# Kernel tuning notes

Hardware: AMD Instinct MI355X
Metric: run time of the kernel (lower is better)

## Reference

```python
import jax, jax.numpy as jnp
import numpy as np

N = 262144  # IMU samples
M = 2048    # synced keyframe poses
GRAVITY = 9.81007

# ---- quaternion helpers (pypose xyzw convention) ----

def qmul(q, r):
    x1, y1, z1, w1 = q[..., 0:1], q[..., 1:2], q[..., 2:3], q[..., 3:4]
    x2, y2, z2, w2 = r[..., 0:1], r[..., 1:2], r[..., 2:3], r[..., 3:4]
    return jnp.concatenate([
        w1 * x2 + x1 * w2 + y1 * z2 - z1 * y2,
        w1 * y2 - x1 * z2 + y1 * w2 + z1 * x2,
        w1 * z2 + x1 * y2 - y1 * x2 + z1 * w2,
        w1 * w2 - x1 * x2 - y1 * y2 - z1 * z2,
    ], axis=-1)


def qconj(q):
    return q * jnp.array([-1.0, -1.0, -1.0, 1.0], dtype=q.dtype)


def qrot(q, v):
    # rotate vector v by unit quaternion q
    xyz, w = q[..., :3], q[..., 3:4]
    t = 2.0 * jnp.cross(xyz, v)
    return v + w * t + jnp.cross(xyz, t)


def exp_so3(phi):
    # axis-angle -> unit quaternion (xyzw); jnp.sinc is safe at 0
    theta = jnp.linalg.norm(phi, axis=-1, keepdims=True)
    half = 0.5 * theta
    xyz = phi * (0.5 * jnp.sinc(half / jnp.pi))  # sin(half)/theta
    w = jnp.cos(half)
    return jnp.concatenate([xyz, w], axis=-1)


def log_so3(q):
    # unit quaternion -> axis-angle vector
    xyz, w = q[..., :3], q[..., 3:4]
    nn = jnp.linalg.norm(xyz, axis=-1, keepdims=True)
    theta = 2.0 * jnp.arctan2(nn, w)
    nn_safe = jnp.maximum(nn, 1e-12)
    scale = jnp.where(nn < 1e-7, 2.0, theta / nn_safe)  # small-angle: ~2*xyz
    return xyz * scale


def preintegrate(accels, gyros, dts, q0, v0, p0):
    """Sequential IMU preintegration (rotation at interval start rotates acc)."""
    grav = jnp.array([0.0, 0.0, -GRAVITY], dtype=accels.dtype)
    dt = dts[:, 0]  # [N]

    def step(carry, inp):
        q, v, p = carry
        w_m, a_m, dti = inp
        a_world = qrot(q, a_m) + grav
        p_new = p + v * dti + 0.5 * a_world * dti * dti
        v_new = v + a_world * dti
        q_new = qmul(q, exp_so3(w_m * dti))
        q_new = q_new / jnp.linalg.norm(q_new)
        return (q_new, v_new, p_new), (q_new, p_new)

    _, (rots, poss) = jax.lax.scan(step, (q0, v0, p0), (gyros, accels, dt))
    return rots, poss  # [N,4], [N,3]


def setup_inputs() -> dict:
    key = jax.random.key(0)
    ks = jax.random.split(key, 11)
    accels = 0.5 * jax.random.normal(ks[0], (N, 3), jnp.float32) \
             + jnp.array([0.0, 0.0, GRAVITY], jnp.float32)
    gyros = 0.1 * jax.random.normal(ks[1], (N, 3), jnp.float32)
    accel_bias = 0.01 * jax.random.normal(ks[2], (3,), jnp.float32)
    gyro_bias = 0.001 * jax.random.normal(ks[3], (3,), jnp.float32)
    dts = 0.004 + 0.002 * jax.random.uniform(ks[4], (N, 1), jnp.float32)  # ~200Hz
    init_rot = jax.random.normal(ks[5], (4,), jnp.float32)
    init_rot = init_rot / jnp.linalg.norm(init_rot)
    init_pos = 0.1 * jax.random.normal(ks[6], (3,), jnp.float32)
    init_vel = 0.1 * jax.random.normal(ks[7], (3,), jnp.float32)
    poses_rot = jax.random.normal(ks[8], (M, 4), jnp.float32)
    poses_rot = poses_rot / jnp.linalg.norm(poses_rot, axis=-1, keepdims=True)
    poses_trans = 10.0 * jax.random.normal(ks[9], (M, 3), jnp.float32)
    sync = jnp.sort(jax.random.randint(ks[10], (M,), 0, N))
    return {"accels": accels, "gyros": gyros, "accel_bias": accel_bias,
            "gyro_bias": gyro_bias, "dts": dts, "init_rot": init_rot,
            "init_pos": init_pos, "init_vel": init_vel,
            "poses_rot": poses_rot, "poses_trans": poses_trans, "sync": sync}


def reference(accels, gyros, accel_bias, gyro_bias, dts, init_rot, init_pos,
              init_vel, poses_rot, poses_trans, sync):
    acc = accels - accel_bias[None, :]
    gyr = gyros - gyro_bias[None, :]
    rots, poss = preintegrate(acc, gyr, dts, init_rot, init_vel, init_pos)
    rot_s = rots[sync]   # [M,4]
    pos_s = poss[sync]   # [M,3]
    rel = qmul(qconj(poses_rot), rot_s)
    roterr = jnp.linalg.norm(log_so3(rel))              # global Frobenius norm
    transerr = jnp.mean((poses_trans - pos_s) ** 2)     # mse_loss
    return roterr + transerr
```

## Files before the change

### kernel.cpp

```cpp
#include <hip/hip_runtime.h>
#include <math.h>

#define NN   262144
#define MM   2048
#define SUB  16
#define BT   64
#define SPB  (BT * SUB)
#define NB1  (NN / SPB)
#define NTH  (NN / SUB)
#define REC  113
#define GRAV 9.81007f

struct Qt { float x, y, z, w; };
struct V3 { float x, y, z; };

__device__ __forceinline__ V3 v3(float x, float y, float z) { V3 r{x, y, z}; return r; }
__device__ __forceinline__ V3 vadd(V3 a, V3 b) { return v3(a.x + b.x, a.y + b.y, a.z + b.z); }
__device__ __forceinline__ V3 vscale(V3 a, float s) { return v3(a.x * s, a.y * s, a.z * s); }
__device__ __forceinline__ float vdot(V3 a, V3 b) { return a.x * b.x + a.y * b.y + a.z * b.z; }

__device__ __forceinline__ Qt qmul(Qt a, Qt b) {
    Qt r;
    r.x = a.w * b.x + a.x * b.w + a.y * b.z - a.z * b.y;
    r.y = a.w * b.y - a.x * b.z + a.y * b.w + a.z * b.x;
    r.z = a.w * b.z + a.x * b.y - a.y * b.x + a.z * b.w;
    r.w = a.w * b.w - a.x * b.x - a.y * b.y - a.z * b.z;
    return r;
}
__device__ __forceinline__ Qt qnorm(Qt a) {
    float rn = rsqrtf(a.x * a.x + a.y * a.y + a.z * a.z + a.w * a.w);
    Qt r{a.x * rn, a.y * rn, a.z * rn, a.w * rn};
    return r;
}
__device__ __forceinline__ V3 qrot(Qt q, V3 v) {
    float tx = 2.f * (q.y * v.z - q.z * v.y);
    float ty = 2.f * (q.z * v.x - q.x * v.z);
    float tz = 2.f * (q.x * v.y - q.y * v.x);
    V3 r;
    r.x = v.x + q.w * tx + (q.y * tz - q.z * ty);
    r.y = v.y + q.w * ty + (q.z * tx - q.x * tz);
    r.z = v.z + q.w * tz + (q.x * ty - q.y * tx);
    return r;
}
__device__ __forceinline__ Qt exp_so3(V3 phi) {
    float t2 = vdot(phi, phi);
    float th = sqrtf(t2);
    float h = 0.5f * th;
    float s, c;
    if (h < 0.1f) {
        float h2 = h * h;
        s = 0.5f * (1.f - h2 * (1.f / 6.f) + h2 * h2 * (1.f / 120.f));
        c = 1.f - h2 * 0.5f + h2 * h2 * (1.f / 24.f);
    } else {
        s = 0.5f * sinf(h) / h;
        c = cosf(h);
    }
    Qt r{phi.x * s, phi.y * s, phi.z * s, c};
    return r;
}

__device__ __forceinline__ void step_state(Qt& q, V3& v, V3& p, V3 a, V3 w, float dt) {
    V3 aw = qrot(q, a);
    aw.z -= GRAV;
    float hdt2 = 0.5f * dt * dt;
    p.x += v.x * dt + aw.x * hdt2;
    p.y += v.y * dt + aw.y * hdt2;
    p.z += v.z * dt + aw.z * hdt2;
    v.x += aw.x * dt;
    v.y += aw.y * dt;
    v.z += aw.z * dt;
    q = qnorm(qmul(q, exp_so3(v3(w.x * dt, w.y * dt, w.z * dt))));
}

struct Sm { Qt q; float T; V3 B1; V3 C; float W; };

__device__ __forceinline__ Sm sm_identity() {
    Sm s; s.q = Qt{0, 0, 0, 1}; s.T = 0; s.B1 = v3(0, 0, 0); s.C = v3(0, 0, 0); s.W = 0; return s;
}
__device__ __forceinline__ Sm sm_combine(const Sm& a, const Sm& b) {
    Sm r;
    r.q  = qnorm(qmul(a.q, b.q));
    r.T  = a.T + b.T;
    r.B1 = vadd(a.B1, qrot(a.q, b.B1));
    r.C  = vadd(vadd(a.C, vscale(a.B1, b.T)), qrot(a.q, b.C));
    r.W  = a.W + a.T * b.T + b.W;
    return r;
}
__device__ __forceinline__ void sm_store(float* p, const Sm& s) {
    p[0] = s.q.x; p[1] = s.q.y; p[2] = s.q.z; p[3] = s.q.w;
    p[4] = s.T;
    p[5] = s.B1.x; p[6] = s.B1.y; p[7] = s.B1.z;
    p[8] = s.C.x;  p[9] = s.C.y;  p[10] = s.C.z;
    p[11] = s.W;
}
__device__ __forceinline__ Sm sm_load(const float* p) {
    Sm s;
    s.q = Qt{p[0], p[1], p[2], p[3]};
    s.T = p[4];
    s.B1 = v3(p[5], p[6], p[7]);
    s.C  = v3(p[8], p[9], p[10]);
    s.W = p[11];
    return s;
}
__device__ __forceinline__ Sm sm_shfl_up(const Sm& s, int off) {
    Sm r;
    r.q.x = __shfl_up(s.q.x, off); r.q.y = __shfl_up(s.q.y, off);
    r.q.z = __shfl_up(s.q.z, off); r.q.w = __shfl_up(s.q.w, off);
    r.T = __shfl_up(s.T, off);
    r.B1.x = __shfl_up(s.B1.x, off); r.B1.y = __shfl_up(s.B1.y, off); r.B1.z = __shfl_up(s.B1.z, off);
    r.C.x = __shfl_up(s.C.x, off);  r.C.y = __shfl_up(s.C.y, off);  r.C.z = __shfl_up(s.C.z, off);
    r.W = __shfl_up(s.W, off);
    return r;
}

struct St { Qt q; V3 v; V3 p; };
__device__ __forceinline__ St apply_sm(const Sm& P, Qt q0, V3 v0, V3 p0) {
    St s;
    s.q = qnorm(qmul(q0, P.q));
    V3 vb = qrot(q0, P.B1);
    V3 pb = qrot(q0, P.C);
    s.v = v3(v0.x + vb.x, v0.y + vb.y, v0.z + vb.z - GRAV * P.T);
    s.p = v3(p0.x + v0.x * P.T + pb.x,
             p0.y + v0.y * P.T + pb.y,
             p0.z + v0.z * P.T + pb.z - GRAV * P.W);
    return s;
}
__device__ __forceinline__ void st_store(float* p, const St& s) {
    p[0] = s.q.x; p[1] = s.q.y; p[2] = s.q.z; p[3] = s.q.w;
    p[4] = s.v.x; p[5] = s.v.y; p[6] = s.v.z;
    p[7] = s.p.x; p[8] = s.p.y; p[9] = s.p.z;
}
__device__ __forceinline__ St st_load(const float* p) {
    St s;
    s.q = Qt{p[0], p[1], p[2], p[3]};
    s.v = v3(p[4], p[5], p[6]);
    s.p = v3(p[7], p[8], p[9]);
    return s;
}

__global__ __launch_bounds__(BT) void k_sum(
    const float* __restrict__ acc, const float* __restrict__ gyr,
    const float* __restrict__ ab, const float* __restrict__ gb,
    const float* __restrict__ dts,
    float* __restrict__ prefix, float* __restrict__ blocksums) {
    __shared__ float lds[BT * REC];
    int b = blockIdx.x;
    int t = threadIdx.x;

    const float4* ga = (const float4*)(acc + (size_t)b * SPB * 3);
    const float4* gg = (const float4*)(gyr + (size_t)b * SPB * 3);
    const float4* gd = (const float4*)(dts + (size_t)b * SPB);
#pragma unroll
    for (int r = 0; r < 12; ++r) {
        int i4 = r * BT + t;
        float4 v = ga[i4];
        int i = i4 * 4;
        float* d = &lds[(i / 48) * REC + (i % 48)];
        d[0] = v.x; d[1] = v.y; d[2] = v.z; d[3] = v.w;
    }
#pragma unroll
    for (int r = 0; r < 12; ++r) {
        int i4 = r * BT + t;
        float4 v = gg[i4];
        int i = i4 * 4;
        float* d = &lds[(i / 48) * REC + 48 + (i % 48)];
        d[0] = v.x; d[1] = v.y; d[2] = v.z; d[3] = v.w;
    }
#pragma unroll
    for (int r = 0; r < 4; ++r) {
        int i4 = r * BT + t;
        float4 v = gd[i4];
        int i = i4 * 4;
        float* d = &lds[(i / 16) * REC + 96 + (i % 16)];
        d[0] = v.x; d[1] = v.y; d[2] = v.z; d[3] = v.w;
    }
    __syncthreads();

    float ab0 = ab[0], ab1 = ab[1], ab2 = ab[2];
    float gb0 = gb[0], gb1 = gb[1], gb2 = gb[2];

    const float* rec = &lds[t * REC];
    Qt q{0.f, 0.f, 0.f, 1.f};
    V3 B1 = v3(0, 0, 0), B2 = v3(0, 0, 0);
    float tt = 0.f, U = 0.f;
#pragma unroll
    for (int j = 0; j < SUB; ++j) {
        V3 a = v3(rec[3 * j] - ab0, rec[3 * j + 1] - ab1, rec[3 * j + 2] - ab2);
        V3 w = v3(rec[48 + 3 * j] - gb0, rec[48 + 3 * j + 1] - gb1, rec[48 + 3 * j + 2] - gb2);
        float dt = rec[96 + j];
        V3 bb = qrot(q, a);
        float tc = tt + 0.5f * dt;
        B1 = vadd(B1, vscale(bb, dt));
        B2 = vadd(B2, vscale(bb, dt * tc));
        U += dt * tc;
        tt += dt;
        q = qnorm(qmul(q, exp_so3(v3(w.x * dt, w.y * dt, w.z * dt))));
    }
    Sm cur;
    cur.q = q; cur.T = tt; cur.B1 = B1;
    cur.C = vadd(vscale(B1, tt), vscale(B2, -1.f));
    cur.W = tt * tt - U;

#pragma unroll
    for (int off = 1; off < 64; off <<= 1) {
        Sm o = sm_shfl_up(cur, off);
        if (t >= off) cur = sm_combine(o, cur);
    }
    sm_store(prefix + (size_t)(b * BT + t) * 12, cur);
    if (t == BT - 1) sm_store(blocksums + (size_t)b * 12, cur);
}

__global__ __launch_bounds__(NB1) void k_scan(
    const float* __restrict__ blocksums,
    const float* __restrict__ q0p, const float* __restrict__ p0p, const float* __restrict__ v0p,
    float* __restrict__ S, float* __restrict__ accum) {
    __shared__ float ls[NB1][12];
    int tid = threadIdx.x;
    Sm cur = sm_load(blocksums + (size_t)tid * 12);
    sm_store(ls[tid], cur);
    for (int off = 1; off < NB1; off <<= 1) {
        __syncthreads();
        Sm t = sm_load(ls[tid]);
        if (tid >= off) t = sm_combine(sm_load(ls[tid - off]), t);
        __syncthreads();
        sm_store(ls[tid], t);
    }
    __syncthreads();
    Qt q0{q0p[0], q0p[1], q0p[2], q0p[3]};
    V3 p0 = v3(p0p[0], p0p[1], p0p[2]);
    V3 v0 = v3(v0p[0], v0p[1], v0p[2]);
    Sm incl = sm_load(ls[tid]);
    St s = apply_sm(incl, q0, v0, p0);
    st_store(S + (size_t)(tid + 1) * 12, s);
    if (tid == 0) {
        St s0; s0.q = qnorm(q0); s0.v = v0; s0.p = p0;
        st_store(S, s0);
        accum[0] = 0.f; accum[1] = 0.f;
    }
}

__global__ __launch_bounds__(64) void k_sync(
    const float* __restrict__ acc, const float* __restrict__ gyr,
    const float* __restrict__ ab, const float* __restrict__ gb,
    const float* __restrict__ dts,
    const float* __restrict__ prefix, const float* __restrict__ S,
    const float* __restrict__ prot, const float* __restrict__ ptrn,
    const int* __restrict__ sync, float* __restrict__ accum) {
    int m = blockIdx.x * blockDim.x + threadIdx.x;
    float rsq = 0.f, tsq = 0.f;
    if (m < MM) {
        int g = sync[m] + 1;
        int b = g >> 10;
        int t = (g >> 4) & (BT - 1);
        int r = g & (SUB - 1);
        St st = st_load(S + (size_t)b * 12);
        if (t > 0) {
            Sm P = sm_load(prefix + (size_t)(b * BT + t - 1) * 12);
            st = apply_sm(P, st.q, st.v, st.p);
        }
        if (r > 0) {
            float ab0 = ab[0], ab1 = ab[1], ab2 = ab[2];
            float gb0 = gb[0], gb1 = gb[1], gb2 = gb[2];
            int base = g & ~(SUB - 1);
            for (int j = 0; j < r; ++j) {
                int i = base + j;
                V3 a = v3(acc[3 * i] - ab0, acc[3 * i + 1] - ab1, acc[3 * i + 2] - ab2);
                V3 w = v3(gyr[3 * i] - gb0, gyr[3 * i + 1] - gb1, gyr[3 * i + 2] - gb2);
                step_state(st.q, st.v, st.p, a, w, dts[i]);
            }
        }
        Qt pr{prot[4 * m], prot[4 * m + 1], prot[4 * m + 2], prot[4 * m + 3]};
        Qt pc{-pr.x, -pr.y, -pr.z, pr.w};
        Qt rel = qmul(pc, st.q);
        float nn = sqrtf(rel.x * rel.x + rel.y * rel.y + rel.z * rel.z);
        float theta = 2.f * atan2f(nn, rel.w);
        float scale = (nn < 1e-7f) ? 2.f : theta / fmaxf(nn, 1e-12f);
        float lx = rel.x * scale, ly = rel.y * scale, lz = rel.z * scale;
        rsq = lx * lx + ly * ly + lz * lz;
        float dx = ptrn[3 * m] - st.p.x, dy = ptrn[3 * m + 1] - st.p.y, dz = ptrn[3 * m + 2] - st.p.z;
        tsq = dx * dx + dy * dy + dz * dz;
    }
    for (int o = 32; o > 0; o >>= 1) {
        rsq += __shfl_down(rsq, o);
        tsq += __shfl_down(tsq, o);
    }
    if ((threadIdx.x & 63) == 0) {
        atomicAdd(&accum[0], rsq);
        atomicAdd(&accum[1], tsq);
    }
}

__global__ void k_fin(const float* __restrict__ accum, float* __restrict__ out) {
    out[0] = sqrtf(accum[0]) + accum[1] * (1.f / (3.f * MM));
}

extern "C" void kernel_launch(void* const* d_in, const int* in_sizes, int n_in,
                              void* d_out, int out_size, void* d_ws, size_t ws_size,
                              hipStream_t stream) {
    const float* acc  = (const float*)d_in[0];
    const float* gyr  = (const float*)d_in[1];
    const float* ab   = (const float*)d_in[2];
    const float* gb   = (const float*)d_in[3];
    const float* dts  = (const float*)d_in[4];
    const float* q0   = (const float*)d_in[5];
    const float* p0   = (const float*)d_in[6];
    const float* v0   = (const float*)d_in[7];
    const float* prot = (const float*)d_in[8];
    const float* ptrn = (const float*)d_in[9];
    const int*   sync = (const int*)d_in[10];

    float* ws     = (float*)d_ws;
    float* prefix = ws;
    float* bsums  = prefix + (size_t)NTH * 12;
    float* S      = bsums + (size_t)NB1 * 12;
    float* accum  = S + (size_t)(NB1 + 1) * 12;
    float* out    = (float*)d_out;

    hipLaunchKernelGGL(k_sum, dim3(NB1), dim3(BT), 0, stream,
                       acc, gyr, ab, gb, dts, prefix, bsums);
    hipLaunchKernelGGL(k_scan, dim3(1), dim3(NB1), 0, stream,
                       bsums, q0, p0, v0, S, accum);
    hipLaunchKernelGGL(k_sync, dim3(MM / 64), dim3(64), 0, stream,
                       acc, gyr, ab, gb, dts, prefix, S, prot, ptrn, sync, accum);
    hipLaunchKernelGGL(k_fin, dim3(1), dim3(1), 0, stream, accum, out);
}
```

Before: 104.4 us.

## Fuse scan, sync-pose evaluation and final reduction into one tail kernel

Merges the block-sum scan, the per-keyframe state reconstruction and the final loss kernel into a single 256-thread block. Block-boundary states now stay in shared memory and the result is reduced in-block, so the global atomics and two kernel launches go away. Quaternion renormalisation is also dropped from each inner step and from the scan combine, normalising only once per 16-sample chunk. The trade-off is that the 2048 keyframes are handled by one block (8 per thread) instead of 32 blocks, and skipping normalisation may cause small numerical drift.

New measurement: 166.9 us. 1.6x slower.

```diff
diff --git a/kernel.cpp b/kernel.cpp
--- a/kernel.cpp
+++ b/kernel.cpp
@@ -74,12 +74,9 @@
 
 struct Sm { Qt q; float T; V3 B1; V3 C; float W; };
 
-__device__ __forceinline__ Sm sm_identity() {
-    Sm s; s.q = Qt{0, 0, 0, 1}; s.T = 0; s.B1 = v3(0, 0, 0); s.C = v3(0, 0, 0); s.W = 0; return s;
-}
 __device__ __forceinline__ Sm sm_combine(const Sm& a, const Sm& b) {
     Sm r;
-    r.q  = qnorm(qmul(a.q, b.q));
+    r.q  = qmul(a.q, b.q);
     r.T  = a.T + b.T;
     r.B1 = vadd(a.B1, qrot(a.q, b.B1));
     r.C  = vadd(vadd(a.C, vscale(a.B1, b.T)), qrot(a.q, b.C));
@@ -194,10 +191,10 @@
         B2 = vadd(B2, vscale(bb, dt * tc));
         U += dt * tc;
         tt += dt;
-        q = qnorm(qmul(q, exp_so3(v3(w.x * dt, w.y * dt, w.z * dt))));
+        q = qmul(q, exp_so3(v3(w.x * dt, w.y * dt, w.z * dt)));
     }
     Sm cur;
-    cur.q = q; cur.T = tt; cur.B1 = B1;
+    cur.q = qnorm(q); cur.T = tt; cur.B1 = B1;
     cur.C = vadd(vscale(B1, tt), vscale(B2, -1.f));
     cur.W = tt * tt - U;
 
@@ -210,12 +207,19 @@
     if (t == BT - 1) sm_store(blocksums + (size_t)b * 12, cur);
 }
 
-__global__ __launch_bounds__(NB1) void k_scan(
-    const float* __restrict__ blocksums,
+__global__ __launch_bounds__(NB1) void k_tail(
+    const float* __restrict__ blocksums, const float* __restrict__ prefix,
+    const float* __restrict__ acc, const float* __restrict__ gyr,
+    const float* __restrict__ ab, const float* __restrict__ gb,
+    const float* __restrict__ dts,
     const float* __restrict__ q0p, const float* __restrict__ p0p, const float* __restrict__ v0p,
-    float* __restrict__ S, float* __restrict__ accum) {
+    const float* __restrict__ prot, const float* __restrict__ ptrn,
+    const int* __restrict__ sync, float* __restrict__ out) {
     __shared__ float ls[NB1][12];
+    __shared__ float Sst[NB1 + 1][12];
+    __shared__ float red_r[4], red_t[4];
     int tid = threadIdx.x;
+
     Sm cur = sm_load(blocksums + (size_t)tid * 12);
     sm_store(ls[tid], cur);
     for (int off = 1; off < NB1; off <<= 1) {
@@ -226,41 +230,34 @@
         sm_store(ls[tid], t);
     }
     __syncthreads();
+
     Qt q0{q0p[0], q0p[1], q0p[2], q0p[3]};
     V3 p0 = v3(p0p[0], p0p[1], p0p[2]);
     V3 v0 = v3(v0p[0], v0p[1], v0p[2]);
-    Sm incl = sm_load(ls[tid]);
-    St s = apply_sm(incl, q0, v0, p0);
-    st_store(S + (size_t)(tid + 1) * 12, s);
+    St s = apply_sm(sm_load(ls[tid]), q0, v0, p0);
+    st_store(Sst[tid + 1], s);
     if (tid == 0) {
         St s0; s0.q = qnorm(q0); s0.v = v0; s0.p = p0;
-        st_store(S, s0);
-        accum[0] = 0.f; accum[1] = 0.f;
-    }
-}
-
-__global__ __launch_bounds__(64) void k_sync(
-    const float* __restrict__ acc, const float* __restrict__ gyr,
-    const float* __restrict__ ab, const float* __restrict__ gb,
-    const float* __restrict__ dts,
-    const float* __restrict__ prefix, const float* __restrict__ S,
-    const float* __restrict__ prot, const float* __restrict__ ptrn,
-    const int* __restrict__ sync, float* __restrict__ accum) {
-    int m = blockIdx.x * blockDim.x + threadIdx.x;
+        st_store(Sst[0], s0);
+    }
+    __syncthreads();
+
+    float ab0 = ab[0], ab1 = ab[1], ab2 = ab[2];
+    float gb0 = gb[0], gb1 = gb[1], gb2 = gb[2];
     float rsq = 0.f, tsq = 0.f;
-    if (m < MM) {
+#pragma unroll
+    for (int k = 0; k < MM / NB1; ++k) {
+        int m = k * NB1 + tid;
         int g = sync[m] + 1;
         int b = g >> 10;
         int t = (g >> 4) & (BT - 1);
         int r = g & (SUB - 1);
-        St st = st_load(S + (size_t)b * 12);
+        St st = st_load(Sst[b]);
         if (t > 0) {
             Sm P = sm_load(prefix + (size_t)(b * BT + t - 1) * 12);
             st = apply_sm(P, st.q, st.v, st.p);
         }
         if (r > 0) {
-            float ab0 = ab[0], ab1 = ab[1], ab2 = ab[2];
-            float gb0 = gb[0], gb1 = gb[1], gb2 = gb[2];
             int base = g & ~(SUB - 1);
             for (int j = 0; j < r; ++j) {
                 int i = base + j;
@@ -276,22 +273,21 @@
         float theta = 2.f * atan2f(nn, rel.w);
         float scale = (nn < 1e-7f) ? 2.f : theta / fmaxf(nn, 1e-12f);
         float lx = rel.x * scale, ly = rel.y * scale, lz = rel.z * scale;
-        rsq = lx * lx + ly * ly + lz * lz;
+        rsq += lx * lx + ly * ly + lz * lz;
         float dx = ptrn[3 * m] - st.p.x, dy = ptrn[3 * m + 1] - st.p.y, dz = ptrn[3 * m + 2] - st.p.z;
-        tsq = dx * dx + dy * dy + dz * dz;
+        tsq += dx * dx + dy * dy + dz * dz;
     }
     for (int o = 32; o > 0; o >>= 1) {
         rsq += __shfl_down(rsq, o);
         tsq += __shfl_down(tsq, o);
     }
-    if ((threadIdx.x & 63) == 0) {
-        atomicAdd(&accum[0], rsq);
-        atomicAdd(&accum[1], tsq);
-    }
-}
-
-__global__ void k_fin(const float* __restrict__ accum, float* __restrict__ out) {
-    out[0] = sqrtf(accum[0]) + accum[1] * (1.f / (3.f * MM));
+    if ((tid & 63) == 0) { red_r[tid >> 6] = rsq; red_t[tid >> 6] = tsq; }
+    __syncthreads();
+    if (tid == 0) {
+        float R = red_r[0] + red_r[1] + red_r[2] + red_r[3];
+        float T = red_t[0] + red_t[1] + red_t[2] + red_t[3];
+        out[0] = sqrtf(R) + T * (1.f / (3.f * MM));
+    }
 }
 
 extern "C" void kernel_launch(void* const* d_in, const int* in_sizes, int n_in,
@@ -312,15 +308,11 @@
     float* ws     = (float*)d_ws;
     float* prefix = ws;
     float* bsums  = prefix + (size_t)NTH * 12;
-    float* S      = bsums + (size_t)NB1 * 12;
-    float* accum  = S + (size_t)(NB1 + 1) * 12;
     float* out    = (float*)d_out;
 
     hipLaunchKernelGGL(k_sum, dim3(NB1), dim3(BT), 0, stream,
                        acc, gyr, ab, gb, dts, prefix, bsums);
-    hipLaunchKernelGGL(k_scan, dim3(1), dim3(NB1), 0, stream,
-                       bsums, q0, p0, v0, S, accum);
-    hipLaunchKernelGGL(k_sync, dim3(MM / 64), dim3(64), 0, stream,
-                       acc, gyr, ab, gb, dts, prefix, S, prot, ptrn, sync, accum);
-    hipLaunchKernelGGL(k_fin, dim3(1), dim3(1), 0, stream, accum, out);
-}
+    hipLaunchKernelGGL(k_tail, dim3(1), dim3(NB1), 0, stream,
+                       bsums, prefix, acc, gyr, ab, gb, dts,
+                       q0, p0, v0, prot, ptrn, sync, out);
+}
```

## Parallelize sync-point tail integration with 16-lane segmented scan

Applied to the files above, without the earlier changes.

The per-keyframe sequential tail loop of up to 15 IMU steps is replaced by 16 lanes per keyframe. Each lane builds a one-sample summary element, and the lanes combine them with a shuffle-based scan before one lane applies the result to the block state. Quaternion renormalization is also dropped from the combine and from the per-sample loop in the summary kernel, leaving a single normalization at the end of each thread's chunk. This cuts serial latency in the sync kernel and some arithmetic in the scans, at the cost of 16x more threads in the sync kernel and possible slight numerical drift.

New measurement: 107.8 us. 3.3% more time.

```diff
diff --git a/kernel.cpp b/kernel.cpp
--- a/kernel.cpp
+++ b/kernel.cpp
@@ -59,32 +59,19 @@
     return r;
 }
 
-__device__ __forceinline__ void step_state(Qt& q, V3& v, V3& p, V3 a, V3 w, float dt) {
-    V3 aw = qrot(q, a);
-    aw.z -= GRAV;
-    float hdt2 = 0.5f * dt * dt;
-    p.x += v.x * dt + aw.x * hdt2;
-    p.y += v.y * dt + aw.y * hdt2;
-    p.z += v.z * dt + aw.z * hdt2;
-    v.x += aw.x * dt;
-    v.y += aw.y * dt;
-    v.z += aw.z * dt;
-    q = qnorm(qmul(q, exp_so3(v3(w.x * dt, w.y * dt, w.z * dt))));
-}
-
 struct Sm { Qt q; float T; V3 B1; V3 C; float W; };
 
-__device__ __forceinline__ Sm sm_identity() {
-    Sm s; s.q = Qt{0, 0, 0, 1}; s.T = 0; s.B1 = v3(0, 0, 0); s.C = v3(0, 0, 0); s.W = 0; return s;
-}
 __device__ __forceinline__ Sm sm_combine(const Sm& a, const Sm& b) {
     Sm r;
-    r.q  = qnorm(qmul(a.q, b.q));
+    r.q  = qmul(a.q, b.q);
     r.T  = a.T + b.T;
     r.B1 = vadd(a.B1, qrot(a.q, b.B1));
     r.C  = vadd(vadd(a.C, vscale(a.B1, b.T)), qrot(a.q, b.C));
     r.W  = a.W + a.T * b.T + b.W;
     return r;
+}
+__device__ __forceinline__ Sm sm_identity() {
+    Sm s; s.q = Qt{0, 0, 0, 1}; s.T = 0; s.B1 = v3(0, 0, 0); s.C = v3(0, 0, 0); s.W = 0; return s;
 }
 __device__ __forceinline__ void sm_store(float* p, const Sm& s) {
     p[0] = s.q.x; p[1] = s.q.y; p[2] = s.q.z; p[3] = s.q.w;
@@ -194,10 +181,10 @@
         B2 = vadd(B2, vscale(bb, dt * tc));
         U += dt * tc;
         tt += dt;
-        q = qnorm(qmul(q, exp_so3(v3(w.x * dt, w.y * dt, w.z * dt))));
+        q = qmul(q, exp_so3(v3(w.x * dt, w.y * dt, w.z * dt)));
     }
     Sm cur;
-    cur.q = q; cur.T = tt; cur.B1 = B1;
+    cur.q = qnorm(q); cur.T = tt; cur.B1 = B1;
     cur.C = vadd(vscale(B1, tt), vscale(B2, -1.f));
     cur.W = tt * tt - U;
 
@@ -229,8 +216,7 @@
     Qt q0{q0p[0], q0p[1], q0p[2], q0p[3]};
     V3 p0 = v3(p0p[0], p0p[1], p0p[2]);
     V3 v0 = v3(v0p[0], v0p[1], v0p[2]);
-    Sm incl = sm_load(ls[tid]);
-    St s = apply_sm(incl, q0, v0, p0);
+    St s = apply_sm(sm_load(ls[tid]), q0, v0, p0);
     st_store(S + (size_t)(tid + 1) * 12, s);
     if (tid == 0) {
         St s0; s0.q = qnorm(q0); s0.v = v0; s0.p = p0;
@@ -240,51 +226,69 @@
 }
 
 __global__ __launch_bounds__(64) void k_sync(
+    const float* __restrict__ prefix, const float* __restrict__ S,
     const float* __restrict__ acc, const float* __restrict__ gyr,
     const float* __restrict__ ab, const float* __restrict__ gb,
     const float* __restrict__ dts,
-    const float* __restrict__ prefix, const float* __restrict__ S,
     const float* __restrict__ prot, const float* __restrict__ ptrn,
     const int* __restrict__ sync, float* __restrict__ accum) {
-    int m = blockIdx.x * blockDim.x + threadIdx.x;
+    int tid = blockIdx.x * 64 + threadIdx.x;
+    int m = tid >> 4;
+    int j = tid & 15;
+
+    int g = sync[m] + 1;
+    int b = g >> 10;
+    int t = (g >> 4) & (BT - 1);
+    int r = g & (SUB - 1);
+
+    St st = st_load(S + (size_t)b * 12);
+    if (t > 0) {
+        Sm P = sm_load(prefix + (size_t)(b * BT + t - 1) * 12);
+        st = apply_sm(P, st.q, st.v, st.p);
+    }
+
+    Sm s;
+    if (j < r) {
+        int i = (g & ~(SUB - 1)) + j;
+        float ab0 = ab[0], ab1 = ab[1], ab2 = ab[2];
+        float gb0 = gb[0], gb1 = gb[1], gb2 = gb[2];
+        V3 a = v3(acc[3 * i] - ab0, acc[3 * i + 1] - ab1, acc[3 * i + 2] - ab2);
+        V3 w = v3(gyr[3 * i] - gb0, gyr[3 * i + 1] - gb1, gyr[3 * i + 2] - gb2);
+        float dt = dts[i];
+        s.q = exp_so3(v3(w.x * dt, w.y * dt, w.z * dt));
+        s.T = dt;
+        s.B1 = vscale(a, dt);
+        s.C  = vscale(a, 0.5f * dt * dt);
+        s.W  = 0.5f * dt * dt;
+    } else {
+        s = sm_identity();
+    }
+
+#pragma unroll
+    for (int off = 1; off < 16; off <<= 1) {
+        Sm o = sm_shfl_up(s, off);
+        if (j >= off) s = sm_combine(o, s);
+    }
+
     float rsq = 0.f, tsq = 0.f;
-    if (m < MM) {
-        int g = sync[m] + 1;
-        int b = g >> 10;
-        int t = (g >> 4) & (BT - 1);
-        int r = g & (SUB - 1);
-        St st = st_load(S + (size_t)b * 12);
-        if (t > 0) {
-            Sm P = sm_load(prefix + (size_t)(b * BT + t - 1) * 12);
-            st = apply_sm(P, st.q, st.v, st.p);
-        }
-        if (r > 0) {
-            float ab0 = ab[0], ab1 = ab[1], ab2 = ab[2];
-            float gb0 = gb[0], gb1 = gb[1], gb2 = gb[2];
-            int base = g & ~(SUB - 1);
-            for (int j = 0; j < r; ++j) {
-                int i = base + j;
-                V3 a = v3(acc[3 * i] - ab0, acc[3 * i + 1] - ab1, acc[3 * i + 2] - ab2);
-                V3 w = v3(gyr[3 * i] - gb0, gyr[3 * i + 1] - gb1, gyr[3 * i + 2] - gb2);
-                step_state(st.q, st.v, st.p, a, w, dts[i]);
-            }
-        }
+    if (j == 15) {
+        St f = apply_sm(s, st.q, st.v, st.p);
         Qt pr{prot[4 * m], prot[4 * m + 1], prot[4 * m + 2], prot[4 * m + 3]};
         Qt pc{-pr.x, -pr.y, -pr.z, pr.w};
-        Qt rel = qmul(pc, st.q);
+        Qt rel = qmul(pc, f.q);
         float nn = sqrtf(rel.x * rel.x + rel.y * rel.y + rel.z * rel.z);
         float theta = 2.f * atan2f(nn, rel.w);
         float scale = (nn < 1e-7f) ? 2.f : theta / fmaxf(nn, 1e-12f);
         float lx = rel.x * scale, ly = rel.y * scale, lz = rel.z * scale;
         rsq = lx * lx + ly * ly + lz * lz;
-        float dx = ptrn[3 * m] - st.p.x, dy = ptrn[3 * m + 1] - st.p.y, dz = ptrn[3 * m + 2] - st.p.z;
+        float dx = ptrn[3 * m] - f.p.x, dy = ptrn[3 * m + 1] - f.p.y, dz = ptrn[3 * m + 2] - f.p.z;
         tsq = dx * dx + dy * dy + dz * dz;
     }
     for (int o = 32; o > 0; o >>= 1) {
         rsq += __shfl_down(rsq, o);
         tsq += __shfl_down(tsq, o);
     }
-    if ((threadIdx.x & 63) == 0) {
+    if (threadIdx.x == 0) {
         atomicAdd(&accum[0], rsq);
         atomicAdd(&accum[1], tsq);
     }
@@ -320,7 +324,7 @@
                        acc, gyr, ab, gb, dts, prefix, bsums);
     hipLaunchKernelGGL(k_scan, dim3(1), dim3(NB1), 0, stream,
                        bsums, q0, p0, v0, S, accum);
-    hipLaunchKernelGGL(k_sync, dim3(MM / 64), dim3(64), 0, stream,
-                       acc, gyr, ab, gb, dts, prefix, S, prot, ptrn, sync, accum);
+    hipLaunchKernelGGL(k_sync, dim3(MM * 16 / 64), dim3(64), 0, stream,
+                       prefix, S, acc, gyr, ab, gb, dts, prot, ptrn, sync, accum);
     hipLaunchKernelGGL(k_fin, dim3(1), dim3(1), 0, stream, accum, out);
 }
```
